# Kernel optimization log

Measured on AMD Instinct MI355X. Metric: run time of the kernel, lower is better.

## Reference

```python
import jax, jax.numpy as jnp
import numpy as np

N_EMBD = 1024
N_HEAD = 16
HEAD_DIM = N_EMBD // N_HEAD
B, T = 2, 2048


def setup_inputs() -> dict:
    key = jax.random.key(0)
    ks = jax.random.split(key, 12)
    s = 0.02
    inp = {
        "x": jax.random.normal(ks[0], (B, T, N_EMBD), dtype=jnp.float32),
        "ln1_g": jnp.ones((N_EMBD,), jnp.float32),
        "ln1_b": jnp.zeros((N_EMBD,), jnp.float32),
        "ln2_g": jnp.ones((N_EMBD,), jnp.float32),
        "ln2_b": jnp.zeros((N_EMBD,), jnp.float32),
        "W_qkv": jax.random.normal(ks[1], (N_EMBD, 3 * N_EMBD), jnp.float32) * s,
        "b_qkv": jnp.zeros((3 * N_EMBD,), jnp.float32),
        "W_o": jax.random.normal(ks[2], (N_EMBD, N_EMBD), jnp.float32) * s,
        "b_o": jnp.zeros((N_EMBD,), jnp.float32),
        "W_fc": jax.random.normal(ks[3], (N_EMBD, 4 * N_EMBD), jnp.float32) * s,
        "b_fc": jnp.zeros((4 * N_EMBD,), jnp.float32),
        "W_proj": jax.random.normal(ks[4], (4 * N_EMBD, N_EMBD), jnp.float32) * s,
        "b_proj": jnp.zeros((N_EMBD,), jnp.float32),
    }
    return inp


def _layernorm(x, g, b, eps=1e-5):
    mu = jnp.mean(x, axis=-1, keepdims=True)
    var = jnp.var(x, axis=-1, keepdims=True)
    return (x - mu) * jax.lax.rsqrt(var + eps) * g + b


def _block(x, ln1_g, ln1_b, ln2_g, ln2_b, W_qkv, b_qkv, W_o, b_o, W_fc, b_fc, W_proj, b_proj):
    # --- attention sub-block (pre-LN) ---
    h = _layernorm(x, ln1_g, ln1_b)
    qkv = h @ W_qkv + b_qkv                     # [B,T,3E]
    q, k, v = jnp.split(qkv, 3, axis=-1)
    def split_heads(t):
        return t.reshape(B, T, N_HEAD, HEAD_DIM).transpose(0, 2, 1, 3)  # [B,H,T,D]
    q, k, v = split_heads(q), split_heads(k), split_heads(v)
    scores = jnp.einsum("bhqd,bhkd->bhqk", q, k) / (HEAD_DIM ** 0.5)
    causal = jnp.tril(jnp.ones((T, T), dtype=bool))
    scores = jnp.where(causal, scores, jnp.float32(-jnp.inf))
    probs = jax.nn.softmax(scores, axis=-1)
    attn = jnp.einsum("bhqk,bhkd->bhqd", probs, v)        # [B,H,T,D]
    attn = attn.transpose(0, 2, 1, 3).reshape(B, T, N_EMBD)
    x = x + attn @ W_o + b_o
    # --- MLP sub-block (pre-LN) ---
    h = _layernorm(x, ln2_g, ln2_b)
    h = jax.nn.gelu(h @ W_fc + b_fc, approximate=False)
    x = x + h @ W_proj + b_proj
    return x


def reference(x, ln1_g, ln1_b, ln2_g, ln2_b, W_qkv, b_qkv, W_o, b_o, W_fc, b_fc, W_proj, b_proj):
    return _block(x, ln1_g, ln1_b, ln2_g, ln2_b, W_qkv, b_qkv, W_o, b_o, W_fc, b_fc, W_proj, b_proj)
```

## Files before the change

kernel.cpp:

```cpp
#include <hip/hip_runtime.h>
#include <hip/hip_bf16.h>


#define TT 2048
#define EE 1024
#define NH 16
#define HD 64

#define AS1 __attribute__((address_space(1)))
#define AS3 __attribute__((address_space(3)))

using bf16x8 = __bf16 __attribute__((ext_vector_type(8)));
using bf16x4 = __bf16 __attribute__((ext_vector_type(4)));
using f32x4  = float __attribute__((ext_vector_type(4)));

template<int N> __device__ __forceinline__ void vm_wait() {
    if constexpr (N == 0)      asm volatile("s_waitcnt vmcnt(0)" ::: "memory");
    else if constexpr (N == 2) asm volatile("s_waitcnt vmcnt(2)" ::: "memory");
    else if constexpr (N == 3) asm volatile("s_waitcnt vmcnt(3)" ::: "memory");
    else if constexpr (N == 4) asm volatile("s_waitcnt vmcnt(4)" ::: "memory");
    else if constexpr (N == 6) asm volatile("s_waitcnt vmcnt(6)" ::: "memory");
    else                       asm volatile("s_waitcnt vmcnt(8)" ::: "memory");
}

__device__ __forceinline__ float gelu_fast(float v) {
    float z  = v * 0.70710678118f;
    float az = fabsf(z);
    float t  = __builtin_amdgcn_rcpf(__builtin_fmaf(0.3275911f, az, 1.0f));
    float p  = t * __builtin_fmaf(t,
                   __builtin_fmaf(t,
                     __builtin_fmaf(t,
                       __builtin_fmaf(t, 1.061405429f, -1.453152027f),
                       1.421413741f),
                     -0.284496736f),
                   0.254829592f);
    float e  = __expf(-az * az);
    float er = copysignf(1.0f - p * e, z);
    return 0.5f * v * (1.0f + er);
}

__global__ __launch_bounds__(256) void convt_kernel(const float* __restrict__ W,
                                                    __bf16* __restrict__ WT,
                                                    int K, int N) {
    __shared__ __bf16 t[32][33];
    int n0 = blockIdx.x * 32, k0 = blockIdx.y * 32;
    int tid = threadIdx.x;
    int r = tid >> 3, c4 = (tid & 7) * 4;
    float4 v = *(const float4*)(W + (size_t)(k0 + r) * N + n0 + c4);
    t[r][c4 + 0] = (__bf16)v.x; t[r][c4 + 1] = (__bf16)v.y;
    t[r][c4 + 2] = (__bf16)v.z; t[r][c4 + 3] = (__bf16)v.w;
    __syncthreads();
    bf16x4 o;
    o[0] = t[c4 + 0][r]; o[1] = t[c4 + 1][r];
    o[2] = t[c4 + 2][r]; o[3] = t[c4 + 3][r];
    *(bf16x4*)(WT + (size_t)(n0 + r) * K + k0 + c4) = o;
}

__global__ __launch_bounds__(256) void convt3_kernel(const float* __restrict__ W0,
                                                     __bf16* __restrict__ T0,
                                                     const float* __restrict__ W1,
                                                     __bf16* __restrict__ T1,
                                                     const float* __restrict__ W2,
                                                     __bf16* __restrict__ T2) {
    __shared__ __bf16 t[32][33];
    int bt = blockIdx.x;
    const float* W; __bf16* WT; int N, nx;
    if (bt < 3072)      {            W = W0; WT = T0; N = 3 * EE; nx = 96;  }
    else if (bt < 4096) { bt -= 3072; W = W1; WT = T1; N = EE;     nx = 32;  }
    else                { bt -= 4096; W = W2; WT = T2; N = 4 * EE; nx = 128; }
    const int K = EE;
    int n0 = (bt % nx) * 32, k0 = (bt / nx) * 32;
    int tid = threadIdx.x;
    int r = tid >> 3, c4 = (tid & 7) * 4;
    float4 v = *(const float4*)(W + (size_t)(k0 + r) * N + n0 + c4);
    t[r][c4 + 0] = (__bf16)v.x; t[r][c4 + 1] = (__bf16)v.y;
    t[r][c4 + 2] = (__bf16)v.z; t[r][c4 + 3] = (__bf16)v.w;
    __syncthreads();
    bf16x4 o;
    o[0] = t[c4 + 0][r]; o[1] = t[c4 + 1][r];
    o[2] = t[c4 + 2][r]; o[3] = t[c4 + 3][r];
    *(bf16x4*)(WT + (size_t)(n0 + r) * K + k0 + c4) = o;
}

__global__ __launch_bounds__(256) void ln_kernel(const float* __restrict__ x,
                                                 const float* __restrict__ g,
                                                 const float* __restrict__ bta,
                                                 __bf16* __restrict__ out) {
    int row = blockIdx.x;
    int tid = threadIdx.x;
    const float4 xv = *(const float4*)(x + (size_t)row * EE + tid * 4);
    float s  = xv.x + xv.y + xv.z + xv.w;
    float ss = xv.x*xv.x + xv.y*xv.y + xv.z*xv.z + xv.w*xv.w;
    __shared__ float rs[256], rss[256];
    rs[tid] = s; rss[tid] = ss;
    __syncthreads();
    for (int st = 128; st > 0; st >>= 1) {
        if (tid < st) { rs[tid] += rs[tid+st]; rss[tid] += rss[tid+st]; }
        __syncthreads();
    }
    float mean = rs[0] * (1.0f / EE);
    float var  = rss[0] * (1.0f / EE) - mean * mean;
    float rstd = rsqrtf(var + 1e-5f);
    const float4 gv = *(const float4*)(g + tid * 4);
    const float4 bv = *(const float4*)(bta + tid * 4);
    bf16x4 ov;
    ov[0] = (__bf16)((xv.x - mean) * rstd * gv.x + bv.x);
    ov[1] = (__bf16)((xv.y - mean) * rstd * gv.y + bv.y);
    ov[2] = (__bf16)((xv.z - mean) * rstd * gv.z + bv.z);
    ov[3] = (__bf16)((xv.w - mean) * rstd * gv.w + bv.w);
    *(bf16x4*)(out + (size_t)row * EE + tid * 4) = ov;
}

template<int TM, int TN, bool GELU, bool RESID, bool QKV, bool ATOMIC, typename CT>
__global__ __launch_bounds__(256) void gemm_bt_kernel(const __bf16* __restrict__ A,
                                                      const __bf16* __restrict__ BT,
                                                      const float* __restrict__ bias,
                                                      const float* resid, CT* C,
                                                      __bf16* vT,
                                                      int M, int N, int K) {
    constexpr int MT = TM / 32;
    constexpr int NT = TN / 32;
    constexpr int LOADS = TM / 64 + TN / 64;
    constexpr int NBUF  = ATOMIC ? 3 : ((LOADS <= 3) ? 4 : 3);
    constexpr int DEPTH = NBUF - 1;
    constexpr int WAITN = (DEPTH - 1) * LOADS;
    __shared__ __align__(16) __bf16 As[NBUF][TM][32];
    __shared__ __align__(16) __bf16 Bs[NBUF][TN][32];
    int tid = threadIdx.x, wave = tid >> 6, lane = tid & 63;
    int quad = lane >> 4, l16 = lane & 15;
    int wm = wave >> 1, wn = wave & 1;

    int NX = (int)gridDim.x, NY = (int)gridDim.y;
    int lin = (int)blockIdx.x + NX * ((int)blockIdx.y + NY * (int)blockIdx.z);
    int total = NX * NY * (int)gridDim.z;
    int g = (lin & 7) * (total >> 3) + (lin >> 3);
    int bx = g % NX;
    int by = (g / NX) % NY;
    int bz = g / (NX * NY);

    int m0 = by * TM, n0 = bx * TN;

    const int klen = ATOMIC ? (K >> 1) : K;
    const int koff = ATOMIC ? bz * klen : 0;

    f32x4 acc[MT][NT] = {};

    int srow = wave * 16 + (lane >> 2);
    int scol = (((lane & 3) ^ ((lane >> 3) & 3)) * 8);
    int xcol = ((quad ^ ((l16 >> 1) & 3)) * 8);

    auto STAGE = [&](int buf, int kt) {
        int kb = koff + (kt << 5);
#pragma unroll
        for (int p = 0; p < TM / 64; p++) {
            const __bf16* gp = A + (size_t)(m0 + p * 64 + srow) * K + kb + scol;
            __builtin_amdgcn_global_load_lds((AS1 const void*)gp,
                                             (AS3 void*)&As[buf][p * 64 + wave * 16][0],
                                             16, 0, 0);
        }
#pragma unroll
        for (int p = 0; p < TN / 64; p++) {
            const __bf16* gp = BT + (size_t)(n0 + p * 64 + srow) * K + kb + scol;
            __builtin_amdgcn_global_load_lds((AS1 const void*)gp,
                                             (AS3 void*)&Bs[buf][p * 64 + wave * 16][0],
                                             16, 0, 0);
        }
    };

    auto COMPUTE = [&](int cur) {
        bf16x8 af[MT], bfr[NT];
#pragma unroll
        for (int mt = 0; mt < MT; mt++)
            af[mt] = *(const bf16x8*)(&As[cur][wm * (MT * 16) + mt * 16 + l16][xcol]);
#pragma unroll
        for (int nt = 0; nt < NT; nt++)
            bfr[nt] = *(const bf16x8*)(&Bs[cur][wn * (NT * 16) + nt * 16 + l16][xcol]);
#pragma unroll
        for (int mt = 0; mt < MT; mt++)
#pragma unroll
            for (int nt = 0; nt < NT; nt++)
                acc[mt][nt] = __builtin_amdgcn_mfma_f32_16x16x32_bf16(af[mt], bfr[nt],
                                                                      acc[mt][nt], 0, 0, 0);
    };

    const int nk = klen >> 5;
#pragma unroll
    for (int i = 0; i < DEPTH; ++i) STAGE(i, i);
    vm_wait<WAITN>();
    __builtin_amdgcn_s_barrier();

    int t = 0;
    for (; t + DEPTH < nk; ++t) {
        STAGE((t + DEPTH) % NBUF, t + DEPTH);
        COMPUTE(t % NBUF);
        vm_wait<WAITN>();
        __builtin_amdgcn_s_barrier();
    }
    for (; t < nk; ++t) {
        COMPUTE(t % NBUF);
        if (t + 1 < nk) {
            int rem = nk - 2 - t;
            if (rem >= 1) vm_wait<LOADS>();
            else          vm_wait<0>();
            __builtin_amdgcn_s_barrier();
        }
    }

#pragma unroll
    for (int nt = 0; nt < NT; nt++) {
        int c = n0 + wn * (NT * 16) + nt * 16 + l16;
        float bv = (!ATOMIC || bz == 0) ? bias[c] : 0.0f;
#pragma unroll
        for (int mt = 0; mt < MT; mt++) {
#pragma unroll
            for (int r = 0; r < 4; r++) {
                int row = m0 + wm * (MT * 16) + mt * 16 + quad * 4 + r;
                float v = acc[mt][nt][r] + bv;
                if (GELU)  v = gelu_fast(v);
                if (RESID) v += resid[(size_t)row * N + c];
                if (ATOMIC) {
                    atomicAdd((float*)&C[(size_t)row * N + c], v);
                } else if (!QKV) {
                    C[(size_t)row * N + c] = (CT)v;
                } else {
                    if (c < 2 * EE) {
                        ((__bf16*)C)[(size_t)row * (2 * EE) + c] = (__bf16)v;
                    } else {
                        int cv = c - 2 * EE;
                        int bb = row >> 11, tt = row & (TT - 1);
                        vT[((size_t)(bb * NH + (cv >> 6)) * HD + (cv & 63)) * TT + tt] =
                            (__bf16)v;
                    }
                }
            }
        }
    }
}

__global__ __launch_bounds__(256) void flash_attn_kernel(const __bf16* __restrict__ qkv,
                                                         const __bf16* __restrict__ vT,
                                                         __bf16* __restrict__ out) {
    int lin = blockIdx.x;
    int xcd = lin & 7, slot = lin >> 3;
    int pair = xcd * 4 + (slot >> 4);
    int qidx = slot & 15;
    int h = pair & 15, b = pair >> 4;

    int tid = threadIdx.x, wave = tid >> 6, lane = tid & 63;
    int quad = lane >> 4, l16 = lane & 15;

    __shared__ __align__(16) __bf16 Ks[128 * 72];
    __shared__ __align__(16) __bf16 Ps[4][16 * 136];

    size_t base = (size_t)b * TT * (2 * EE);

    int srow = tid >> 3;
    int scol = (tid & 7) * 8;
    const __bf16* kbase  = qkv + base + EE + h * HD + scol;
    const __bf16* vrow = vT + (size_t)(b * NH + h) * HD * TT + (size_t)l16 * TT + quad * 8;
    __bf16* Psw = &Ps[wave][0];

    for (int pass = 0; pass < 2; pass++) {
        int qt = pass == 0 ? (31 - qidx) : qidx;
        int q0 = qt * 64;

        int qrow = q0 + wave * 16 + l16;
        const __bf16* qp = qkv + base + (size_t)qrow * (2 * EE) + h * HD;
        bf16x8 aq0 = *(const bf16x8*)(qp + quad * 8);
        bf16x8 aq1 = *(const bf16x8*)(qp + 32 + quad * 8);

        f32x4 oacc[4] = {};
        float lsum[4] = {0.f, 0.f, 0.f, 0.f};
        int qg_base = q0 + wave * 16 + quad * 4;

        int nIter = (qt >> 1) + 1;

        bf16x8 kr[4];
#pragma unroll
        for (int p = 0; p < 4; p++)
            kr[p] = *(const bf16x8*)(kbase + (size_t)(32 * p + srow) * (2 * EE));

        for (int kt = 0; kt < nIter; ++kt) {
            int k0 = kt * 128;
#pragma unroll
            for (int p = 0; p < 4; p++)
                *(bf16x8*)(&Ks[(32 * p + srow) * 72 + scol]) = kr[p];
            __syncthreads();

            bf16x8 vf[4][4];
#pragma unroll
            for (int dt = 0; dt < 4; dt++)
#pragma unroll
                for (int w = 0; w < 4; w++)
                    vf[dt][w] = *(const bf16x8*)(vrow + (size_t)dt * (16 * TT) + k0 + w * 32);

            if (kt < nIter - 1) {
                int kn = k0 + 128;
#pragma unroll
                for (int p = 0; p < 4; p++)
                    kr[p] = *(const bf16x8*)(kbase + (size_t)(kn + 32 * p + srow) * (2 * EE));
            }

            f32x4 s[8];
            __builtin_amdgcn_s_setprio(1);
#pragma unroll
            for (int nt = 0; nt < 8; nt++) {
                bf16x8 bk0 = *(const bf16x8*)(&Ks[(nt * 16 + l16) * 72 + quad * 8]);
                bf16x8 bk1 = *(const bf16x8*)(&Ks[(nt * 16 + l16) * 72 + 32 + quad * 8]);
                f32x4 z = {};
                z = __builtin_amdgcn_mfma_f32_16x16x32_bf16(aq0, bk0, z, 0, 0, 0);
                s[nt] = __builtin_amdgcn_mfma_f32_16x16x32_bf16(aq1, bk1, z, 0, 0, 0);
            }
            __builtin_amdgcn_s_setprio(0);

            bool maskt = (kt == nIter - 1);
#pragma unroll
            for (int nt = 0; nt < 8; nt++) {
                int key = k0 + nt * 16 + l16;
                int cb = 2 * nt + (l16 >> 3);
#pragma unroll
                for (int r = 0; r < 4; r++) {
                    float p;
                    if (maskt && key > qg_base + r) p = 0.0f;
                    else p = __expf(fminf(s[nt][r] * 0.125f, 30.0f));
                    lsum[r] += p;
                    int q = quad * 4 + r;
                    int col = (((cb & 8) | ((cb - 2 * q) & 7)) << 3) | (l16 & 7);
                    Psw[q * 136 + col] = (__bf16)p;
                }
            }

            __builtin_amdgcn_s_setprio(1);
#pragma unroll
            for (int w = 0; w < 4; w++) {
                int cbr = 4 * w + quad;
                int colr = ((cbr & 8) | ((cbr - 2 * l16) & 7)) << 3;
                bf16x8 ap = *(const bf16x8*)(&Psw[l16 * 136 + colr]);
#pragma unroll
                for (int dt = 0; dt < 4; dt++)
                    oacc[dt] = __builtin_amdgcn_mfma_f32_16x16x32_bf16(ap, vf[dt][w],
                                                                       oacc[dt], 0, 0, 0);
            }
            __builtin_amdgcn_s_setprio(0);
            __syncthreads();
        }

#pragma unroll
        for (int off = 1; off < 16; off <<= 1)
#pragma unroll
            for (int r = 0; r < 4; r++) lsum[r] += __shfl_xor(lsum[r], off);
#pragma unroll
        for (int dt = 0; dt < 4; dt++) {
#pragma unroll
            for (int r = 0; r < 4; r++) {
                int qg = qg_base + r;
                out[((size_t)b * TT + qg) * EE + h * HD + dt * 16 + l16] =
                    (__bf16)(oacc[dt][r] / lsum[r]);
            }
        }
    }
}

extern "C" void kernel_launch(void* const* d_in, const int* in_sizes, int n_in,
                              void* d_out, int out_size, void* d_ws, size_t ws_size,
                              hipStream_t stream) {
    const float* x     = (const float*)d_in[0];
    const float* ln1g  = (const float*)d_in[1];
    const float* ln1b  = (const float*)d_in[2];
    const float* ln2g  = (const float*)d_in[3];
    const float* ln2b  = (const float*)d_in[4];
    const float* Wqkv  = (const float*)d_in[5];
    const float* bqkv  = (const float*)d_in[6];
    const float* Wo    = (const float*)d_in[7];
    const float* bo    = (const float*)d_in[8];
    const float* Wfc   = (const float*)d_in[9];
    const float* bfc   = (const float*)d_in[10];
    const float* Wproj = (const float*)d_in[11];
    const float* bproj = (const float*)d_in[12];
    float* out = (float*)d_out;

    const int M = 2 * TT;

    __bf16* ws = (__bf16*)d_ws;
    __bf16* regQ   = ws;
    __bf16* regS   = ws + 16777216;
    __bf16* WfcT   = ws + 20971520;
    __bf16* qkv    = regQ;
    __bf16* vT     = regQ + 8388608;
    __bf16* WqkvT  = regQ + 12582912;
    __bf16* WoT    = regQ + 15728640;
    __bf16* ff     = regQ;
    __bf16* h1 = regS, *atn = regS, *h2 = regS;
    __bf16* WprojT = regS;
    float*  x1 = out;

    convt3_kernel<<<8192, 256, 0, stream>>>(Wqkv, WqkvT, Wo, WoT, Wfc, WfcT);

    ln_kernel<<<M, 256, 0, stream>>>(x, ln1g, ln1b, h1);
    gemm_bt_kernel<128, 128, false, false, true, false, __bf16>
        <<<dim3(3 * EE / 128, M / 128), 256, 0, stream>>>(
        h1, WqkvT, bqkv, nullptr, qkv, vT, M, 3 * EE, EE);
    flash_attn_kernel<<<512, 256, 0, stream>>>(qkv, vT, atn);
    gemm_bt_kernel<128, 64, false, true, false, false, float>
        <<<dim3(EE / 64, M / 128), 256, 0, stream>>>(
        atn, WoT, bo, x, x1, nullptr, M, EE, EE);
    ln_kernel<<<M, 256, 0, stream>>>(x1, ln2g, ln2b, h2);
    gemm_bt_kernel<128, 128, true, false, false, false, __bf16>
        <<<dim3(4 * EE / 128, M / 128), 256, 0, stream>>>(
        h2, WfcT, bfc, nullptr, ff, nullptr, M, 4 * EE, EE);
    convt_kernel<<<dim3(EE / 32, 4 * EE / 32), 256, 0, stream>>>(Wproj, WprojT, 4 * EE, EE);
    gemm_bt_kernel<128, 64, false, false, false, true, float>
        <<<dim3(EE / 64, M / 128, 2), 256, 0, stream>>>(
        ff, WprojT, bproj, nullptr, out, nullptr, M, EE, 4 * EE);
}
```

Baseline: 417.7 us.

## Split attention into one q-tile per block, use wave-shuffle LayerNorm reduction

```diff
diff --git a/kernel.cpp b/kernel.cpp
--- a/kernel.cpp
+++ b/kernel.cpp
@@ -87,19 +87,22 @@
                                                  const float* __restrict__ bta,
                                                  __bf16* __restrict__ out) {
     int row = blockIdx.x;
-    int tid = threadIdx.x;
+    int tid = threadIdx.x, wave = tid >> 6, lane = tid & 63;
     const float4 xv = *(const float4*)(x + (size_t)row * EE + tid * 4);
     float s  = xv.x + xv.y + xv.z + xv.w;
     float ss = xv.x*xv.x + xv.y*xv.y + xv.z*xv.z + xv.w*xv.w;
-    __shared__ float rs[256], rss[256];
-    rs[tid] = s; rss[tid] = ss;
+#pragma unroll
+    for (int off = 32; off > 0; off >>= 1) {
+        s  += __shfl_xor(s, off);
+        ss += __shfl_xor(ss, off);
+    }
+    __shared__ float wsum[8];
+    if (lane == 0) { wsum[wave] = s; wsum[wave + 4] = ss; }
     __syncthreads();
-    for (int st = 128; st > 0; st >>= 1) {
-        if (tid < st) { rs[tid] += rs[tid+st]; rss[tid] += rss[tid+st]; }
-        __syncthreads();
-    }
-    float mean = rs[0] * (1.0f / EE);
-    float var  = rss[0] * (1.0f / EE) - mean * mean;
+    s  = wsum[0] + wsum[1] + wsum[2] + wsum[3];
+    ss = wsum[4] + wsum[5] + wsum[6] + wsum[7];
+    float mean = s * (1.0f / EE);
+    float var  = ss * (1.0f / EE) - mean * mean;
     float rstd = rsqrtf(var + 1e-5f);
     const float4 gv = *(const float4*)(g + tid * 4);
     const float4 bv = *(const float4*)(bta + tid * 4);
@@ -241,9 +244,11 @@
                                                          const __bf16* __restrict__ vT,
                                                          __bf16* __restrict__ out) {
     int lin = blockIdx.x;
-    int xcd = lin & 7, slot = lin >> 3;
-    int pair = xcd * 4 + (slot >> 4);
-    int qidx = slot & 15;
+    int xcd = lin & 7;
+    int s_  = lin >> 3;
+    int hb  = s_ & 3;
+    int qt  = 31 - (s_ >> 2);
+    int pair = xcd * 4 + hb;
     int h = pair & 15, b = pair >> 4;
 
     int tid = threadIdx.x, wave = tid >> 6, lane = tid & 63;
@@ -260,103 +265,100 @@
     const __bf16* vrow = vT + (size_t)(b * NH + h) * HD * TT + (size_t)l16 * TT + quad * 8;
     __bf16* Psw = &Ps[wave][0];
 
-    for (int pass = 0; pass < 2; pass++) {
-        int qt = pass == 0 ? (31 - qidx) : qidx;
-        int q0 = qt * 64;
-
-        int qrow = q0 + wave * 16 + l16;
-        const __bf16* qp = qkv + base + (size_t)qrow * (2 * EE) + h * HD;
-        bf16x8 aq0 = *(const bf16x8*)(qp + quad * 8);
-        bf16x8 aq1 = *(const bf16x8*)(qp + 32 + quad * 8);
-
-        f32x4 oacc[4] = {};
-        float lsum[4] = {0.f, 0.f, 0.f, 0.f};
-        int qg_base = q0 + wave * 16 + quad * 4;
-
-        int nIter = (qt >> 1) + 1;
-
-        bf16x8 kr[4];
+    int q0 = qt * 64;
+
+    int qrow = q0 + wave * 16 + l16;
+    const __bf16* qp = qkv + base + (size_t)qrow * (2 * EE) + h * HD;
+    bf16x8 aq0 = *(const bf16x8*)(qp + quad * 8);
+    bf16x8 aq1 = *(const bf16x8*)(qp + 32 + quad * 8);
+
+    f32x4 oacc[4] = {};
+    float lsum[4] = {0.f, 0.f, 0.f, 0.f};
+    int qg_base = q0 + wave * 16 + quad * 4;
+
+    int nIter = (qt >> 1) + 1;
+
+    bf16x8 kr[4];
+#pragma unroll
+    for (int p = 0; p < 4; p++)
+        kr[p] = *(const bf16x8*)(kbase + (size_t)(32 * p + srow) * (2 * EE));
+
+    for (int kt = 0; kt < nIter; ++kt) {
+        int k0 = kt * 128;
 #pragma unroll
         for (int p = 0; p < 4; p++)
-            kr[p] = *(const bf16x8*)(kbase + (size_t)(32 * p + srow) * (2 * EE));
-
-        for (int kt = 0; kt < nIter; ++kt) {
-            int k0 = kt * 128;
+            *(bf16x8*)(&Ks[(32 * p + srow) * 72 + scol]) = kr[p];
+        __syncthreads();
+
+        bf16x8 vf[4][4];
+#pragma unroll
+        for (int dt = 0; dt < 4; dt++)
+#pragma unroll
+            for (int w = 0; w < 4; w++)
+                vf[dt][w] = *(const bf16x8*)(vrow + (size_t)dt * (16 * TT) + k0 + w * 32);
+
+        if (kt < nIter - 1) {
+            int kn = k0 + 128;
 #pragma unroll
             for (int p = 0; p < 4; p++)
-                *(bf16x8*)(&Ks[(32 * p + srow) * 72 + scol]) = kr[p];
-            __syncthreads();
-
-            bf16x8 vf[4][4];
+                kr[p] = *(const bf16x8*)(kbase + (size_t)(kn + 32 * p + srow) * (2 * EE));
+        }
+
+        f32x4 s[8];
+        __builtin_amdgcn_s_setprio(1);
+#pragma unroll
+        for (int nt = 0; nt < 8; nt++) {
+            bf16x8 bk0 = *(const bf16x8*)(&Ks[(nt * 16 + l16) * 72 + quad * 8]);
+            bf16x8 bk1 = *(const bf16x8*)(&Ks[(nt * 16 + l16) * 72 + 32 + quad * 8]);
+            f32x4 z = {};
+            z = __builtin_amdgcn_mfma_f32_16x16x32_bf16(aq0, bk0, z, 0, 0, 0);
+            s[nt] = __builtin_amdgcn_mfma_f32_16x16x32_bf16(aq1, bk1, z, 0, 0, 0);
+        }
+        __builtin_amdgcn_s_setprio(0);
+
+        bool maskt = (kt == nIter - 1);
+#pragma unroll
+        for (int nt = 0; nt < 8; nt++) {
+            int key = k0 + nt * 16 + l16;
+            int cb = 2 * nt + (l16 >> 3);
+#pragma unroll
+            for (int r = 0; r < 4; r++) {
+                float p;
+                if (maskt && key > qg_base + r) p = 0.0f;
+                else p = exp2f(fminf(s[nt][r] * 0.180336880f, 43.28085f));
+                lsum[r] += p;
+                int q = quad * 4 + r;
+                int col = (((cb & 8) | ((cb - 2 * q) & 7)) << 3) | (l16 & 7);
+                Psw[q * 136 + col] = (__bf16)p;
+            }
+        }
+
+        __builtin_amdgcn_s_setprio(1);
+#pragma unroll
+        for (int w = 0; w < 4; w++) {
+            int cbr = 4 * w + quad;
+            int colr = ((cbr & 8) | ((cbr - 2 * l16) & 7)) << 3;
+            bf16x8 ap = *(const bf16x8*)(&Psw[l16 * 136 + colr]);
 #pragma unroll
             for (int dt = 0; dt < 4; dt++)
-#pragma unroll
-                for (int w = 0; w < 4; w++)
-                    vf[dt][w] = *(const bf16x8*)(vrow + (size_t)dt * (16 * TT) + k0 + w * 32);
-
-            if (kt < nIter - 1) {
-                int kn = k0 + 128;
-#pragma unroll
-                for (int p = 0; p < 4; p++)
-                    kr[p] = *(const bf16x8*)(kbase + (size_t)(kn + 32 * p + srow) * (2 * EE));
-            }
-
-            f32x4 s[8];
-            __builtin_amdgcn_s_setprio(1);
-#pragma unroll
-            for (int nt = 0; nt < 8; nt++) {
-                bf16x8 bk0 = *(const bf16x8*)(&Ks[(nt * 16 + l16) * 72 + quad * 8]);
-                bf16x8 bk1 = *(const bf16x8*)(&Ks[(nt * 16 + l16) * 72 + 32 + quad * 8]);
-                f32x4 z = {};
-                z = __builtin_amdgcn_mfma_f32_16x16x32_bf16(aq0, bk0, z, 0, 0, 0);
-                s[nt] = __builtin_amdgcn_mfma_f32_16x16x32_bf16(aq1, bk1, z, 0, 0, 0);
-            }
-            __builtin_amdgcn_s_setprio(0);
-
-            bool maskt = (kt == nIter - 1);
-#pragma unroll
-            for (int nt = 0; nt < 8; nt++) {
-                int key = k0 + nt * 16 + l16;
-                int cb = 2 * nt + (l16 >> 3);
-#pragma unroll
-                for (int r = 0; r < 4; r++) {
-                    float p;
-                    if (maskt && key > qg_base + r) p = 0.0f;
-                    else p = __expf(fminf(s[nt][r] * 0.125f, 30.0f));
-                    lsum[r] += p;
-                    int q = quad * 4 + r;
-                    int col = (((cb & 8) | ((cb - 2 * q) & 7)) << 3) | (l16 & 7);
-                    Psw[q * 136 + col] = (__bf16)p;
-                }
-            }
-
-            __builtin_amdgcn_s_setprio(1);
-#pragma unroll
-            for (int w = 0; w < 4; w++) {
-                int cbr = 4 * w + quad;
-                int colr = ((cbr & 8) | ((cbr - 2 * l16) & 7)) << 3;
-                bf16x8 ap = *(const bf16x8*)(&Psw[l16 * 136 + colr]);
-#pragma unroll
-                for (int dt = 0; dt < 4; dt++)
-                    oacc[dt] = __builtin_amdgcn_mfma_f32_16x16x32_bf16(ap, vf[dt][w],
-                                                                       oacc[dt], 0, 0, 0);
-            }
-            __builtin_amdgcn_s_setprio(0);
-            __syncthreads();
-        }
-
-#pragma unroll
-        for (int off = 1; off < 16; off <<= 1)
-#pragma unroll
-            for (int r = 0; r < 4; r++) lsum[r] += __shfl_xor(lsum[r], off);
-#pragma unroll
-        for (int dt = 0; dt < 4; dt++) {
-#pragma unroll
-            for (int r = 0; r < 4; r++) {
-                int qg = qg_base + r;
-                out[((size_t)b * TT + qg) * EE + h * HD + dt * 16 + l16] =
-                    (__bf16)(oacc[dt][r] / lsum[r]);
-            }
+                oacc[dt] = __builtin_amdgcn_mfma_f32_16x16x32_bf16(ap, vf[dt][w],
+                                                                   oacc[dt], 0, 0, 0);
+        }
+        __builtin_amdgcn_s_setprio(0);
+        __syncthreads();
+    }
+
+#pragma unroll
+    for (int off = 1; off < 16; off <<= 1)
+#pragma unroll
+        for (int r = 0; r < 4; r++) lsum[r] += __shfl_xor(lsum[r], off);
+#pragma unroll
+    for (int dt = 0; dt < 4; dt++) {
+#pragma unroll
+        for (int r = 0; r < 4; r++) {
+            int qg = qg_base + r;
+            out[((size_t)b * TT + qg) * EE + h * HD + dt * 16 + l16] =
+                (__bf16)(oacc[dt][r] / lsum[r]);
         }
     }
 }
@@ -400,7 +402,7 @@
     gemm_bt_kernel<128, 128, false, false, true, false, __bf16>
         <<<dim3(3 * EE / 128, M / 128), 256, 0, stream>>>(
         h1, WqkvT, bqkv, nullptr, qkv, vT, M, 3 * EE, EE);
-    flash_attn_kernel<<<512, 256, 0, stream>>>(qkv, vT, atn);
+    flash_attn_kernel<<<1024, 256, 0, stream>>>(qkv, vT, atn);
     gemm_bt_kernel<128, 64, false, true, false, false, float>
         <<<dim3(EE / 64, M / 128), 256, 0, stream>>>(
         atn, WoT, bo, x, x1, nullptr, M, EE, EE);
```

Result: no change. 414.7 us (-0.7%).
